# Performance work log

Hardware: AMD Instinct MI355X
Metric: run time of the kernel (lower is better)

Reference implementation:

```python
import jax, jax.numpy as jnp
import numpy as np
from jax import lax

B, D, N, K, POOL = 256, 512, 50000, 32, 1024
ALPHA, BETA, LAMB = 1.0, 1.0, 1e-4
TAU, EPS, DELTA = 0.1, 0.1, 1e-3
SINKHORN_ITERS = 200


def matrix_sqrt(A):
    # differentiable symmetric PSD matrix sqrt via eigendecomposition
    w, v = jnp.linalg.eigh(A)
    w = jnp.clip(w, 0.0)
    return (v * jnp.sqrt(w)) @ v.T


def ridge_cov(M, delta):
    Dm = M.shape[0]
    S = M + (jnp.trace(M) / Dm * delta) * jnp.eye(Dm, dtype=M.dtype)
    return 0.5 * (S + S.T)


def sinkhorn(p, q, C, eps):
    # entropic OT, fixed-iteration Sinkhorn (ot.sinkhorn equivalent)
    Kmat = jnp.exp(-C / eps)
    def step(uv, _):
        u, v = uv
        u = p / (Kmat @ v + 1e-16)
        v = q / (Kmat.T @ u + 1e-16)
        return (u, v), None
    (u, v), _ = lax.scan(step, (jnp.ones_like(p), jnp.ones_like(q)), None, length=SINKHORN_ITERS)
    return u[:, None] * Kmat * v[None, :]


def setup_inputs():
    key = jax.random.key(0)
    k1, k2, k3, k4, k5, k6 = jax.random.split(key, 6)
    return {
        "q_batch": jax.random.normal(k1, (B, D), jnp.float32),
        "q_indices": jax.random.randint(k2, (B,), 0, POOL),
        "W": jax.random.normal(k3, (D, D), jnp.float32) * 0.05,
        "X": jax.random.normal(k4, (N, D), jnp.float32),
        "pre_indices": jax.random.randint(k5, (POOL, K), 0, N),
        "pre_weights": jax.random.uniform(k6, (POOL, K), jnp.float32, 0.1, 1.0),
    }


def _forward(q_batch, W, X, pre_weights, q_indices, pre_indices):
    T = q_batch @ W  # model := single linear layer, T_q_batch [B, D]
    # ---- distribution alignment (2-Wasserstein between Gaussians) ----
    mu_X = X.mean(0)
    Sigma_X = ridge_cov(jnp.cov(X, rowvar=False).astype(X.dtype), DELTA)
    mu_t = T.mean(0)
    Sigma_t = ridge_cov(jnp.cov(T, rowvar=False).astype(T.dtype), max(DELTA, 1e-4))
    term_mean = jnp.sum((mu_t - mu_X) ** 2)
    s_t = matrix_sqrt(Sigma_t)
    M = s_t @ Sigma_X @ s_t
    s_m = matrix_sqrt(0.5 * (M + M.T))
    term_cov = jnp.trace(Sigma_X + Sigma_t - 2.0 * s_m)
    loss_dist = term_mean + jnp.clip(term_cov, 0.0)
    # ---- kNN consistency with entropic OT ----
    T_sg = lax.stop_gradient(T)  # faiss search is on detached queries
    d2 = (T_sg ** 2).sum(1, keepdims=True) - 2.0 * T_sg @ X.T + (X ** 2).sum(1)[None, :]
    _, post_idx = lax.top_k(-d2, K)  # exact brute-force kNN == faiss IndexFlatL2
    Xn = X[post_idx]  # [B, K, D]
    l2 = ((T[:, None, :] - Xn) ** 2).sum(-1)  # [B, K], grads flow through T
    post_w = jax.nn.softmax(-l2 / TAU, axis=1)
    post_w = jnp.clip(post_w, 1e-8)
    post_w = post_w / post_w.sum(1, keepdims=True)
    pre_idx_b = pre_indices[q_indices]  # [B, K]
    pre_w = jnp.clip(pre_weights[q_indices], 1e-8)
    pre_w = pre_w / pre_w.sum(1, keepdims=True)
    # fixed-size support = concat(pre, post) of size 2K; duplicated points cost 0
    # to move between, so OT value matches the deduped-union formulation
    support = jnp.concatenate([pre_idx_b, post_idx], axis=1)  # [B, 2K]
    S = X[support]  # [B, 2K, D]
    sq = (S ** 2).sum(-1)
    C = jnp.clip(sq[:, :, None] + sq[:, None, :] - 2.0 * jnp.einsum('bid,bjd->bij', S, S), 0.0)
    med = jnp.median(C.reshape(C.shape[0], -1), axis=1)
    C = C / (med[:, None, None] + 1e-8)
    zeros = jnp.zeros_like(pre_w)
    p = jnp.concatenate([pre_w, zeros], axis=1)   # pre mass on first K slots
    q = jnp.concatenate([zeros, post_w], axis=1)  # post mass on last K slots
    plans = jax.vmap(lambda pp, qq, cc: sinkhorn(pp, qq, cc, EPS))(p, q, C)
    loss_knn = (plans * C).sum((1, 2)).mean()
    loss_reg = 0.5 * jnp.sum(W ** 2)
    total = ALPHA * loss_dist + BETA * loss_knn + LAMB * loss_reg
    return total, loss_dist, loss_knn


def reference(q_batch, q_indices, W, X, pre_indices, pre_weights):
    return _forward(q_batch, W, X, pre_weights, q_indices, pre_indices)
```

## Files before the change

kernel.cpp:

```cpp
#include <hip/hip_runtime.h>
#include <float.h>
#include <math.h>

#define BB 256
#define DD 512
#define NN 50000
#define KK 32
#define NS_ITERS 11
#define PARTS 8
#define PCH 6250

#define OFF_G     0
#define OFF_SC    262144
#define OFF_CS    262208
#define OFF_CSS   262720
#define ZERO_F    263232
#define OFF_T     263232
#define OFF_TC    394304
#define OFF_P     525376
#define OFF_H     656448
#define OFF_XSQ   723008
#define OFF_RUNI  781200
#define OFF_PW    789392
#define OFF_PRW   797584
#define OFF_D2    805776

#define OFF_UUT   (OFF_G)
#define OFF_TCTC  (OFF_G + 65536)
#define OFF_W     (OFF_G + 131072)
#define OFF_M     (OFF_G + 131328)
#define OFF_MUT   (OFF_G + 200000)

typedef __attribute__((ext_vector_type(8))) short bf16x8;
typedef __attribute__((ext_vector_type(4))) float f32x4;

__device__ __forceinline__ float waveSum(float v) {
#pragma unroll
  for (int off = 32; off > 0; off >>= 1) v += __shfl_xor(v, off);
  return v;
}

__device__ __forceinline__ void cvt_write(float4 v, unsigned short* hi, unsigned short* lo, int sa) {
  unsigned int b0 = __float_as_uint(v.x), b1 = __float_as_uint(v.y);
  unsigned int b2 = __float_as_uint(v.z), b3 = __float_as_uint(v.w);
  unsigned int h0 = b0 & 0xffff0000u, h1 = b1 & 0xffff0000u;
  unsigned int h2 = b2 & 0xffff0000u, h3 = b3 & 0xffff0000u;
  float l0 = v.x - __uint_as_float(h0), l1 = v.y - __uint_as_float(h1);
  float l2 = v.z - __uint_as_float(h2), l3 = v.w - __uint_as_float(h3);
  *(unsigned int*)&hi[sa]     = (h0 >> 16) | h1;
  *(unsigned int*)&hi[sa + 2] = (h2 >> 16) | h3;
  *(unsigned int*)&lo[sa]     = (__float_as_uint(l0) >> 16) | (__float_as_uint(l1) & 0xffff0000u);
  *(unsigned int*)&lo[sa + 2] = (__float_as_uint(l2) >> 16) | (__float_as_uint(l3) & 0xffff0000u);
}

__device__ __forceinline__ void cvt1(float x, unsigned short* hp, unsigned short* lp) {
  unsigned int bb = __float_as_uint(x);
  unsigned int hb = bb & 0xffff0000u;
  float lo = x - __uint_as_float(hb);
  *hp = (unsigned short)(hb >> 16);
  *lp = (unsigned short)(__float_as_uint(lo) >> 16);
}

__global__ void __launch_bounds__(256) k_g64_nn(const float* __restrict__ A,
                                                const float* __restrict__ B,
                                                float* __restrict__ C,
                                                int K, int lda, int ldb, int ldc, float scale,
                                                float* __restrict__ musum) {
  __shared__ float As[64][65], Bs[64][65];
  __shared__ float cp[64];
  int m0 = blockIdx.y * 64, n0 = blockIdx.x * 64;
  int t = threadIdx.x, tr = t >> 4, tc = t & 15;
  float acc[4][4] = {{0.f}};
  for (int k0 = 0; k0 < K; k0 += 64) {
#pragma unroll
    for (int p = 0; p < 16; ++p) {
      int l = t + 256 * p;
      int r = l >> 6, c = l & 63;
      As[r][c] = A[(m0 + r) * lda + k0 + c];
      Bs[r][c] = B[(k0 + r) * ldb + n0 + c];
    }
    __syncthreads();
#pragma unroll 16
    for (int kk = 0; kk < 64; ++kk) {
      float a[4], b[4];
#pragma unroll
      for (int u = 0; u < 4; ++u) a[u] = As[tr + 16 * u][kk];
#pragma unroll
      for (int v = 0; v < 4; ++v) b[v] = Bs[kk][tc + 16 * v];
#pragma unroll
      for (int u = 0; u < 4; ++u)
#pragma unroll
        for (int v = 0; v < 4; ++v) acc[u][v] += a[u] * b[v];
    }
    __syncthreads();
  }
#pragma unroll
  for (int u = 0; u < 4; ++u)
#pragma unroll
    for (int v = 0; v < 4; ++v)
      C[(m0 + tr + 16 * u) * ldc + n0 + tc + 16 * v] = acc[u][v] * scale;
  if (musum != nullptr) {
    if (t < 64) cp[t] = 0.f;
    __syncthreads();
#pragma unroll
    for (int v = 0; v < 4; ++v) {
      float s = 0.f;
#pragma unroll
      for (int u = 0; u < 4; ++u) s += acc[u][v];
      atomicAdd(&cp[tc + 16 * v], s * scale);
    }
    __syncthreads();
    if (t < 64) atomicAdd(&musum[n0 + t], cp[t]);
  }
}

__global__ void __launch_bounds__(256) k_g64_nt(const float* __restrict__ A,
                                                const float* __restrict__ B,
                                                float* __restrict__ C,
                                                int K, int lda, int ldb, int ldc, float scale) {
  __shared__ float As[64][65], Bs[64][65];
  int m0 = blockIdx.y * 64, n0 = blockIdx.x * 64;
  int t = threadIdx.x, tr = t >> 4, tc = t & 15;
  float acc[4][4] = {{0.f}};
  for (int k0 = 0; k0 < K; k0 += 64) {
#pragma unroll
    for (int p = 0; p < 16; ++p) {
      int l = t + 256 * p;
      int r = l >> 6, c = l & 63;
      As[r][c] = A[(m0 + r) * lda + k0 + c];
      Bs[r][c] = B[(n0 + r) * ldb + k0 + c];
    }
    __syncthreads();
#pragma unroll 16
    for (int kk = 0; kk < 64; ++kk) {
      float a[4], b[4];
#pragma unroll
      for (int u = 0; u < 4; ++u) a[u] = As[tr + 16 * u][kk];
#pragma unroll
      for (int v = 0; v < 4; ++v) b[v] = Bs[tc + 16 * v][kk];
#pragma unroll
      for (int u = 0; u < 4; ++u)
#pragma unroll
        for (int v = 0; v < 4; ++v) acc[u][v] += a[u] * b[v];
    }
    __syncthreads();
  }
#pragma unroll
  for (int u = 0; u < 4; ++u)
#pragma unroll
    for (int v = 0; v < 4; ++v)
      C[(m0 + tr + 16 * u) * ldc + n0 + tc + 16 * v] = acc[u][v] * scale;
}

__global__ void __launch_bounds__(256) k_vgemm(const float* __restrict__ T,
                                               const float* __restrict__ X,
                                               float* __restrict__ V,
                                               float* __restrict__ m) {
  __shared__ unsigned short Ah[128 * 72], Al[128 * 72], Bh[128 * 72], Bl[128 * 72];
  __shared__ float colpart[128];
  int bj = blockIdx.x, bi = blockIdx.y;
  int t = threadIdx.x;
  int wave = t >> 6, lane = t & 63;
  int m0 = (wave >> 1) * 64, n0 = (wave & 1) * 64;
  int lrow = lane & 15, lq = lane >> 4;
  int r_ = t >> 4, c4_ = (t & 15) * 4;
  f32x4 acc[4][4] = {};
  float4 pa[8], pb[8];
#pragma unroll
  for (int f = 0; f < 8; ++f) {
    int r = f * 16 + r_;
    pa[f] = *(const float4*)&T[(bi * 128 + r) * 512 + c4_];
    int jg = bj * 128 + r;
    float4 vb = {0.f, 0.f, 0.f, 0.f};
    if (jg < NN) vb = *(const float4*)&X[(size_t)jg * 512 + c4_];
    pb[f] = vb;
  }
  for (int kc = 0; kc < 512; kc += 64) {
#pragma unroll
    for (int f = 0; f < 8; ++f) {
      int sa = (f * 16 + r_) * 72 + c4_;
      cvt_write(pa[f], Ah, Al, sa);
      cvt_write(pb[f], Bh, Bl, sa);
    }
    __syncthreads();
    if (kc < 448) {
      int kn = kc + 64;
#pragma unroll
      for (int f = 0; f < 8; ++f) {
        int r = f * 16 + r_;
        pa[f] = *(const float4*)&T[(bi * 128 + r) * 512 + kn + c4_];
        int jg = bj * 128 + r;
        float4 vb = {0.f, 0.f, 0.f, 0.f};
        if (jg < NN) vb = *(const float4*)&X[(size_t)jg * 512 + kn + c4_];
        pb[f] = vb;
      }
    }
#pragma unroll
    for (int ks = 0; ks < 2; ++ks) {
      int kb = ks * 32 + lq * 8;
      bf16x8 ah[4], al[4], bh[4], bl[4];
#pragma unroll
      for (int mi = 0; mi < 4; ++mi) {
        int ro = (m0 + mi * 16 + lrow) * 72 + kb;
        ah[mi] = *(const bf16x8*)&Ah[ro];
        al[mi] = *(const bf16x8*)&Al[ro];
      }
#pragma unroll
      for (int nj = 0; nj < 4; ++nj) {
        int ro = (n0 + nj * 16 + lrow) * 72 + kb;
        bh[nj] = *(const bf16x8*)&Bh[ro];
        bl[nj] = *(const bf16x8*)&Bl[ro];
      }
#pragma unroll
      for (int mi = 0; mi < 4; ++mi)
#pragma unroll
        for (int nj = 0; nj < 4; ++nj) {
          acc[mi][nj] = __builtin_amdgcn_mfma_f32_16x16x32_bf16(ah[mi], bh[nj], acc[mi][nj], 0, 0, 0);
          acc[mi][nj] = __builtin_amdgcn_mfma_f32_16x16x32_bf16(ah[mi], bl[nj], acc[mi][nj], 0, 0, 0);
          acc[mi][nj] = __builtin_amdgcn_mfma_f32_16x16x32_bf16(al[mi], bh[nj], acc[mi][nj], 0, 0, 0);
        }
    }
    __syncthreads();
  }
  if (t < 128) colpart[t] = 0.f;
  __syncthreads();
#pragma unroll
  for (int mi = 0; mi < 4; ++mi)
#pragma unroll
    for (int nj = 0; nj < 4; ++nj)
#pragma unroll
      for (int r = 0; r < 4; ++r) {
        int row = bi * 128 + m0 + mi * 16 + lq * 4 + r;
        int col = bj * 128 + n0 + nj * 16 + lrow;
        if (col < NN) V[(size_t)row * NN + col] = acc[mi][nj][r];
      }
#pragma unroll
  for (int nj = 0; nj < 4; ++nj) {
    float s = 0.f;
#pragma unroll
    for (int mi = 0; mi < 4; ++mi)
#pragma unroll
      for (int r = 0; r < 4; ++r) s += acc[mi][nj][r];
    atomicAdd(&colpart[n0 + nj * 16 + lrow], s);
  }
  __syncthreads();
  if (t < 128) {
    int col = bj * 128 + t;
    if (col < NN) atomicAdd(&m[col], colpart[t] * (1.0f / 256.0f));
  }
}

__global__ void __launch_bounds__(256) k_uut(const float* __restrict__ V,
                                             const float* __restrict__ m,
                                             float* __restrict__ UUT) {
  __shared__ unsigned short Ah[128 * 72], Al[128 * 72], Bh[128 * 72], Bl[128 * 72];
  __shared__ __align__(16) float ms[1000];
  const int pi_[3] = {0, 0, 1}, pj_[3] = {0, 1, 1};
  int bi = pi_[blockIdx.x], bj = pj_[blockIdx.x];
  bool diag = (bi == bj);
  int j0 = blockIdx.y * 1000, jlim = j0 + 1000;
  int t = threadIdx.x;
  int wave = t >> 6, lane = t & 63;
  int m0 = (wave >> 1) * 64, n0 = (wave & 1) * 64;
  int lrow = lane & 15, lq = lane >> 4;
  int r_ = t >> 4, c4_ = (t & 15) * 4;
  f32x4 acc[4][4] = {};
  if (t < 250) ((float4*)ms)[t] = *(const float4*)&m[j0 + t * 4];
  float4 pa[8], pb[8];
#pragma unroll
  for (int f = 0; f < 8; ++f) {
    int r = f * 16 + r_;
    int jb = j0 + c4_;
    float4 va = {0.f, 0.f, 0.f, 0.f}, vb = {0.f, 0.f, 0.f, 0.f};
    if (jb < jlim) {
      va = *(const float4*)&V[(size_t)(bi * 128 + r) * NN + jb];
      if (!diag) vb = *(const float4*)&V[(size_t)(bj * 128 + r) * NN + jb];
    }
    pa[f] = va; pb[f] = vb;
  }
  __syncthreads();
  const unsigned short* BhP = diag ? (const unsigned short*)Ah : (const unsigned short*)Bh;
  const unsigned short* BlP = diag ? (const unsigned short*)Al : (const unsigned short*)Bl;
  for (int ch = 0; ch < 16; ++ch) {
    int jc = j0 + ch * 64;
#pragma unroll
    for (int f = 0; f < 8; ++f) {
      int sa = (f * 16 + r_) * 72 + c4_;
      int jb = jc + c4_;
      float4 va = pa[f], vb = pb[f];
      if (jb < jlim) {
        float4 mm = *(const float4*)&ms[jb - j0];
        va.x -= mm.x; va.y -= mm.y; va.z -= mm.z; va.w -= mm.w;
        if (!diag) { vb.x -= mm.x; vb.y -= mm.y; vb.z -= mm.z; vb.w -= mm.w; }
      }
      cvt_write(va, Ah, Al, sa);
      if (!diag) cvt_write(vb, Bh, Bl, sa);
    }
    __syncthreads();
    if (ch < 15) {
      int jn = j0 + (ch + 1) * 64;
#pragma unroll
      for (int f = 0; f < 8; ++f) {
        int r = f * 16 + r_;
        int jb = jn + c4_;
        float4 va = {0.f, 0.f, 0.f, 0.f}, vb = {0.f, 0.f, 0.f, 0.f};
        if (jb < jlim) {
          va = *(const float4*)&V[(size_t)(bi * 128 + r) * NN + jb];
          if (!diag) vb = *(const float4*)&V[(size_t)(bj * 128 + r) * NN + jb];
        }
        pa[f] = va; pb[f] = vb;
      }
    }
#pragma unroll
    for (int ks = 0; ks < 2; ++ks) {
      int kb = ks * 32 + lq * 8;
      bf16x8 ah[4], al[4], bh[4], bl[4];
#pragma unroll
      for (int mi = 0; mi < 4; ++mi) {
        int ro = (m0 + mi * 16 + lrow) * 72 + kb;
        ah[mi] = *(const bf16x8*)&Ah[ro];
        al[mi] = *(const bf16x8*)&Al[ro];
      }
#pragma unroll
      for (int nj = 0; nj < 4; ++nj) {
        int ro = (n0 + nj * 16 + lrow) * 72 + kb;
        bh[nj] = *(const bf16x8*)&BhP[ro];
        bl[nj] = *(const bf16x8*)&BlP[ro];
      }
#pragma unroll
      for (int mi = 0; mi < 4; ++mi)
#pragma unroll
        for (int nj = 0; nj < 4; ++nj) {
          acc[mi][nj] = __builtin_amdgcn_mfma_f32_16x16x32_bf16(ah[mi], bh[nj], acc[mi][nj], 0, 0, 0);
          acc[mi][nj] = __builtin_amdgcn_mfma_f32_16x16x32_bf16(ah[mi], bl[nj], acc[mi][nj], 0, 0, 0);
          acc[mi][nj] = __builtin_amdgcn_mfma_f32_16x16x32_bf16(al[mi], bh[nj], acc[mi][nj], 0, 0, 0);
        }
    }
    __syncthreads();
  }
#pragma unroll
  for (int mi = 0; mi < 4; ++mi)
#pragma unroll
    for (int nj = 0; nj < 4; ++nj)
#pragma unroll
      for (int r = 0; r < 4; ++r) {
        int row = bi * 128 + m0 + mi * 16 + lq * 4 + r;
        int col = bj * 128 + n0 + nj * 16 + lrow;
        atomicAdd(&UUT[row * 256 + col], acc[mi][nj][r]);
      }
}

__global__ void __launch_bounds__(256) k_colstatX(const float* __restrict__ X, float* __restrict__ colsum,
                                                  float* __restrict__ colss, float* __restrict__ xsq) {
  __shared__ float shs[512], shq[512];
  int b = blockIdx.x, t = threadIdx.x;
  int wave = t >> 6, lane = t & 63;
  shs[t] = 0.f; shq[t] = 0.f; shs[t + 256] = 0.f; shq[t + 256] = 0.f;
  __syncthreads();
  int c0 = lane * 4;
  float s0 = 0, s1 = 0, s2 = 0, s3 = 0, s4 = 0, s5 = 0, s6 = 0, s7 = 0;
  float q0 = 0, q1 = 0, q2 = 0, q3 = 0, q4 = 0, q5 = 0, q6 = 0, q7 = 0;
  int r0 = b * 200 + wave * 50;
  for (int rr = 0; rr < 50; ++rr) {
    const float* Xr = X + (size_t)(r0 + rr) * 512;
    float4 a = *(const float4*)&Xr[c0];
    float4 c = *(const float4*)&Xr[c0 + 256];
    s0 += a.x; s1 += a.y; s2 += a.z; s3 += a.w;
    s4 += c.x; s5 += c.y; s6 += c.z; s7 += c.w;
    float ax = a.x * a.x, ay = a.y * a.y, az = a.z * a.z, aw = a.w * a.w;
    float cx = c.x * c.x, cy = c.y * c.y, cz = c.z * c.z, cw = c.w * c.w;
    q0 += ax; q1 += ay; q2 += az; q3 += aw;
    q4 += cx; q5 += cy; q6 += cz; q7 += cw;
    float rsq = waveSum(((ax + ay) + (az + aw)) + ((cx + cy) + (cz + cw)));
    if (lane == 0) xsq[r0 + rr] = rsq;
  }
  atomicAdd(&shs[c0 + 0], s0); atomicAdd(&shs[c0 + 1], s1);
  atomicAdd(&shs[c0 + 2], s2); atomicAdd(&shs[c0 + 3], s3);
  atomicAdd(&shs[c0 + 256], s4); atomicAdd(&shs[c0 + 257], s5);
  atomicAdd(&shs[c0 + 258], s6); atomicAdd(&shs[c0 + 259], s7);
  atomicAdd(&shq[c0 + 0], q0); atomicAdd(&shq[c0 + 1], q1);
  atomicAdd(&shq[c0 + 2], q2); atomicAdd(&shq[c0 + 3], q3);
  atomicAdd(&shq[c0 + 256], q4); atomicAdd(&shq[c0 + 257], q5);
  atomicAdd(&shq[c0 + 258], q6); atomicAdd(&shq[c0 + 259], q7);
  __syncthreads();
  atomicAdd(&colsum[t], shs[t]);             atomicAdd(&colss[t], shq[t]);
  atomicAdd(&colsum[t + 256], shs[t + 256]); atomicAdd(&colss[t + 256], shq[t + 256]);
}

__global__ void k_centerT(const float* __restrict__ T, const float* __restrict__ mu,
                          float* __restrict__ Tc, float* __restrict__ scal) {
  __shared__ float red[4];
  int t = threadIdx.x;
  int base = blockIdx.x * 1024;
  float ss = 0.f;
#pragma unroll
  for (int p = 0; p < 4; ++p) {
    int l = base + p * 256 + t;
    float v = T[l] - mu[l & 511] * (1.0f / 256.0f);
    Tc[l] = v;
    ss += v * v;
  }
  ss = waveSum(ss);
  if ((t & 63) == 0) red[t >> 6] = ss;
  __syncthreads();
  if (t == 0) atomicAdd(&scal[0], red[0] + red[1] + red[2] + red[3]);
}

__global__ void k_trCX(const float* __restrict__ colsum, const float* __restrict__ colss,
                       float* __restrict__ scal) {
  __shared__ float red[8];
  int t = threadIdx.x;
  float mu = colsum[t] * (1.0f / 50000.0f);
  float v = (colss[t] - 50000.0f * mu * mu) * (1.0f / 49999.0f);
  v = waveSum(v);
  if ((t & 63) == 0) red[t >> 6] = v;
  __syncthreads();
  if (t == 0) {
    float s = 0;
    for (int i = 0; i < 8; ++i) s += red[i];
    scal[1] = s;
  }
}

__global__ void __launch_bounds__(256) k_wvec(const float* __restrict__ T,
                                              const float* __restrict__ colsum,
                                              float* __restrict__ w, float* __restrict__ scal) {
  __shared__ float cs[512];
  int t = threadIdx.x, lane = t & 63, wv_ = t >> 6;
  cs[t] = colsum[t] * (1.0f / 50000.0f);
  cs[t + 256] = colsum[t + 256] * (1.0f / 50000.0f);
  __syncthreads();
  int rbase = blockIdx.x * 32 + wv_ * 8;
  float tot = 0.f;
  for (int rr = 0; rr < 8; ++rr) {
    int row = rbase + rr;
    float a = 0.f;
#pragma unroll
    for (int d = 0; d < 8; ++d) a += T[row * 512 + lane + 64 * d] * cs[lane + 64 * d];
    a = waveSum(a);
    if (lane == 0) { w[row] = a; tot += a; }
  }
  if (lane == 0) atomicAdd(&scal[6], tot);
}

__global__ void k_hfix(const float* __restrict__ UUT, const float* __restrict__ TcTc,
                       const float* __restrict__ w, const float* __restrict__ scal,
                       float* __restrict__ H) {
  int l = blockIdx.x * 256 + threadIdx.x;
  int i = l >> 8, j = l & 255;
  float u = (i >= 128 && j < 128) ? UUT[j * 256 + i] : UUT[i * 256 + j];
  float rho = scal[1] * (1e-3f / 512.0f);
  float wm = scal[6] * (1.0f / 256.0f);
  float wi = w[i] - wm, wj = w[j] - wm;
  H[l] = (u - 50000.0f * wi * wj) * (1.0f / (49999.0f * 255.0f))
       + rho * TcTc[i * 256 + j] * (1.0f / 255.0f);
}

__global__ void __launch_bounds__(256) k_power(const float* __restrict__ H,
                                               float* __restrict__ scal) {
  __shared__ float v[256], nv[256], red[4];
  int t = threadIdx.x;
  float rt = scal[0] * (1.0f / 255.0f) * (1e-3f / 512.0f);
  v[t] = 1.0f;
  __syncthreads();
  float n2 = 256.0f, n3 = 256.0f;
  for (int it = 0; it < 3; ++it) {
    float s = rt * v[t];
    for (int j = 0; j < 256; ++j) s += H[j * 256 + t] * v[j];
    nv[t] = s;
    float ss = waveSum(s * s);
    if ((t & 63) == 0) red[t >> 6] = ss;
    __syncthreads();
    float norm2 = red[0] + red[1] + red[2] + red[3];
    if (it == 1) n2 = norm2;
    if (it == 2) n3 = norm2;
    v[t] = nv[t];
    __syncthreads();
  }
  float d = H[t * 256 + t] + rt;
#pragma unroll
  for (int off = 32; off > 0; off >>= 1) d = fmaxf(d, __shfl_xor(d, off));
  if ((t & 63) == 0) red[t >> 6] = d;
  __syncthreads();
  if (t == 0) {
    float lam = sqrtf(n3 / n2);
    float md = fmaxf(fmaxf(red[0], red[1]), fmaxf(red[2], red[3]));
    scal[5] = fmaxf(1.3f * lam, md);
  }
}

__global__ void k_nsinit(const float* __restrict__ H, const float* __restrict__ scal,
                         float* __restrict__ Y, float* __restrict__ Z) {
  int l = blockIdx.x * 256 + threadIdx.x;
  int i = l >> 8, j = l & 255;
  float rt = scal[0] * (1.0f / 255.0f) * (1e-3f / 512.0f);
  float inv = 1.0f / scal[5];
  Y[l] = (H[l] + ((i == j) ? rt : 0.f)) * inv;
  Z[l] = (i == j) ? 1.0f : 0.f;
}

__device__ __forceinline__ void ns_mfma_tile(const float* __restrict__ A, const float* __restrict__ B,
                                             const float* __restrict__ D, float* __restrict__ O,
                                             int m0b, int n0b, float dscale, float ascale,
                                             unsigned short* Ah, unsigned short* Al,
                                             unsigned short* Bh, unsigned short* Bl) {
  int t = threadIdx.x, wave = t >> 6, lane = t & 63;
  int m0 = (wave >> 1) * 32, n0 = (wave & 1) * 32;
  int lrow = lane & 15, lq = lane >> 4;
  f32x4 acc[2][2] = {};
  for (int k0 = 0; k0 < 256; k0 += 64) {
#pragma unroll
    for (int f = 0; f < 4; ++f) {
      int lin = f * 256 + t;
      int r = lin >> 4, c4 = (lin & 15) * 4;
      float4 va = *(const float4*)&A[(m0b + r) * 256 + k0 + c4];
      cvt_write(va, Ah, Al, r * 72 + c4);
      float4 vb = *(const float4*)&B[(k0 + r) * 256 + n0b + c4];
      cvt1(vb.x, &Bh[(c4 + 0) * 72 + r], &Bl[(c4 + 0) * 72 + r]);
      cvt1(vb.y, &Bh[(c4 + 1) * 72 + r], &Bl[(c4 + 1) * 72 + r]);
      cvt1(vb.z, &Bh[(c4 + 2) * 72 + r], &Bl[(c4 + 2) * 72 + r]);
      cvt1(vb.w, &Bh[(c4 + 3) * 72 + r], &Bl[(c4 + 3) * 72 + r]);
    }
    __syncthreads();
#pragma unroll
    for (int ks = 0; ks < 2; ++ks) {
      int kb = ks * 32 + lq * 8;
      bf16x8 ah[2], al2[2], bh[2], bl2[2];
#pragma unroll
      for (int mi = 0; mi < 2; ++mi) {
        int ro = (m0 + mi * 16 + lrow) * 72 + kb;
        ah[mi] = *(const bf16x8*)&Ah[ro];
        al2[mi] = *(const bf16x8*)&Al[ro];
      }
#pragma unroll
      for (int nj = 0; nj < 2; ++nj) {
        int ro = (n0 + nj * 16 + lrow) * 72 + kb;
        bh[nj] = *(const bf16x8*)&Bh[ro];
        bl2[nj] = *(const bf16x8*)&Bl[ro];
      }
#pragma unroll
      for (int mi = 0; mi < 2; ++mi)
#pragma unroll
        for (int nj = 0; nj < 2; ++nj) {
          acc[mi][nj] = __builtin_amdgcn_mfma_f32_16x16x32_bf16(ah[mi], bh[nj], acc[mi][nj], 0, 0, 0);
          acc[mi][nj] = __builtin_amdgcn_mfma_f32_16x16x32_bf16(ah[mi], bl2[nj], acc[mi][nj], 0, 0, 0);
          acc[mi][nj] = __builtin_amdgcn_mfma_f32_16x16x32_bf16(al2[mi], bh[nj], acc[mi][nj], 0, 0, 0);
        }
    }
    __syncthreads();
  }
#pragma unroll
  for (int mi = 0; mi < 2; ++mi)
#pragma unroll
    for (int nj = 0; nj < 2; ++nj)
#pragma unroll
      for (int r = 0; r < 4; ++r) {
        int row = m0b + m0 + mi * 16 + lq * 4 + r;
        int col = n0b + n0 + nj * 16 + lrow;
        int idx = row * 256 + col;
        float base = (dscale != 0.f) ? dscale * D[idx] : 0.f;
        O[idx] = base + ascale * acc[mi][nj][r];
      }
}

__global__ void __launch_bounds__(256) k_nsp(const float* __restrict__ Z,
                                             const float* __restrict__ Y,
                                             float* __restrict__ P) {
  __shared__ unsigned short Ah[64 * 72], Al[64 * 72], Bh[64 * 72], Bl[64 * 72];
  ns_mfma_tile(Z, Y, Z, P, blockIdx.y * 64, blockIdx.x * 64, 0.f, 1.0f, Ah, Al, Bh, Bl);
}

__global__ void __launch_bounds__(256) k_nsu(const float* __restrict__ Y, const float* __restrict__ Z,
                                             const float* __restrict__ Pm,
                                             float* __restrict__ Yn, float* __restrict__ Zn) {
  __shared__ unsigned short Ah[64 * 72], Al[64 * 72], Bh[64 * 72], Bl[64 * 72];
  int zz = blockIdx.z;
  if (zz == 0)
    ns_mfma_tile(Y, Pm, Y, Yn, blockIdx.y * 64, blockIdx.x * 64, 1.5f, -0.5f, Ah, Al, Bh, Bl);
  else
    ns_mfma_tile(Pm, Z, Z, Zn, blockIdx.y * 64, blockIdx.x * 64, 1.5f, -0.5f, Ah, Al, Bh, Bl);
}

__global__ void __launch_bounds__(256) k_nsu_diag(const float* __restrict__ Y,
                                                  const float* __restrict__ Pm,
                                                  float* __restrict__ scal) {
  __shared__ unsigned short Ah[64 * 72], Al[64 * 72], Bh[64 * 72], Bl[64 * 72];
  __shared__ float red[4];
  int bi = blockIdx.x;
  int m0b = bi * 64, n0b = bi * 64;
  int t = threadIdx.x, wave = t >> 6, lane = t & 63;
  int m0 = (wave >> 1) * 32, n0 = (wave & 1) * 32;
  int lrow = lane & 15, lq = lane >> 4;
  f32x4 acc[2][2] = {};
  for (int k0 = 0; k0 < 256; k0 += 64) {
#pragma unroll
    for (int f = 0; f < 4; ++f) {
      int lin = f * 256 + t;
      int r = lin >> 4, c4 = (lin & 15) * 4;
      float4 va = *(const float4*)&Y[(m0b + r) * 256 + k0 + c4];
      cvt_write(va, Ah, Al, r * 72 + c4);
      float4 vb = *(const float4*)&Pm[(k0 + r) * 256 + n0b + c4];
      cvt1(vb.x, &Bh[(c4 + 0) * 72 + r], &Bl[(c4 + 0) * 72 + r]);
      cvt1(vb.y, &Bh[(c4 + 1) * 72 + r], &Bl[(c4 + 1) * 72 + r]);
      cvt1(vb.z, &Bh[(c4 + 2) * 72 + r], &Bl[(c4 + 2) * 72 + r]);
      cvt1(vb.w, &Bh[(c4 + 3) * 72 + r], &Bl[(c4 + 3) * 72 + r]);
    }
    __syncthreads();
#pragma unroll
    for (int ks = 0; ks < 2; ++ks) {
      int kb = ks * 32 + lq * 8;
      bf16x8 ah[2], al2[2], bh[2], bl2[2];
#pragma unroll
      for (int mi = 0; mi < 2; ++mi) {
        int ro = (m0 + mi * 16 + lrow) * 72 + kb;
        ah[mi] = *(const bf16x8*)&Ah[ro];
        al2[mi] = *(const bf16x8*)&Al[ro];
      }
#pragma unroll
      for (int nj = 0; nj < 2; ++nj) {
        int ro = (n0 + nj * 16 + lrow) * 72 + kb;
        bh[nj] = *(const bf16x8*)&Bh[ro];
        bl2[nj] = *(const bf16x8*)&Bl[ro];
      }
#pragma unroll
      for (int mi = 0; mi < 2; ++mi)
#pragma unroll
        for (int nj = 0; nj < 2; ++nj) {
          acc[mi][nj] = __builtin_amdgcn_mfma_f32_16x16x32_bf16(ah[mi], bh[nj], acc[mi][nj], 0, 0, 0);
          acc[mi][nj] = __builtin_amdgcn_mfma_f32_16x16x32_bf16(ah[mi], bl2[nj], acc[mi][nj], 0, 0, 0);
          acc[mi][nj] = __builtin_amdgcn_mfma_f32_16x16x32_bf16(al2[mi], bh[nj], acc[mi][nj], 0, 0, 0);
        }
    }
    __syncthreads();
  }
  float lacc = 0.f;
#pragma unroll
  for (int mi = 0; mi < 2; ++mi)
#pragma unroll
    for (int nj = 0; nj < 2; ++nj)
#pragma unroll
      for (int r = 0; r < 4; ++r) {
        int row = m0 + mi * 16 + lq * 4 + r;
        int col = n0 + nj * 16 + lrow;
        if (row == col)
          lacc += 1.5f * Y[(m0b + row) * 256 + n0b + col] - 0.5f * acc[mi][nj][r];
      }
  lacc = waveSum(lacc);
  if ((t & 63) == 0) red[t >> 6] = lacc;
  __syncthreads();
  if (t == 0) atomicAdd(&scal[7], red[0] + red[1] + red[2] + red[3]);
}

__global__ void __launch_bounds__(256) k_topk_part(const float* __restrict__ V,
                                                   const float* __restrict__ xsq,
                                                   float* __restrict__ candv,
                                                   int* __restrict__ candi) {
  __shared__ float bufv[512];
  __shared__ int bufi[512];
  __shared__ int lcount;
  __shared__ float tvs;
  __shared__ int tis;
  int part = blockIdx.x, q = blockIdx.y, t = threadIdx.x;
  int base = part * PCH;
  int lane = t & 63;
  if (t == 0) { lcount = 0; tvs = FLT_MAX; tis = 0x7fffffff; }
  __syncthreads();
  const float* rowV = V + (size_t)q * NN + base;
  const float* xs = xsq + base;

  auto flush = [&]() {
    __syncthreads();
    int c = lcount;
    for (int s = c + t; s < 512; s += 256) { bufv[s] = FLT_MAX; bufi[s] = 0x7fffffff; }
    __syncthreads();
    for (int ssz = 2; ssz <= 512; ssz <<= 1) {
      for (int st = ssz >> 1; st > 0; st >>= 1) {
        int i = 2 * t - (t & (st - 1));
        int j = i + st;
        bool up = ((i & ssz) == 0);
        float a = bufv[i], b = bufv[j];
        int ai = bufi[i], bi2 = bufi[j];
        bool agtb = (a > b) || (a == b && ai > bi2);
        if (agtb == up) { bufv[i] = b; bufv[j] = a; bufi[i] = bi2; bufi[j] = ai; }
        __syncthreads();
      }
    }
    if (t == 0) { lcount = 32; tvs = bufv[31]; tis = bufi[31]; }
    __syncthreads();
  };

  int ntile = (PCH + 255) >> 8;
  for (int tile = 0; tile < ntile; ++tile) {
    int j = tile * 256 + t;
    float val = 0.f; int idx = 0;
    bool pred = false;
    if (j < PCH) {
      val = xs[j] - 2.0f * rowV[j];
      idx = base + j;
      float tv = tvs; int ti = tis;
      pred = (val < tv) || (val == tv && idx < ti);
    }
    unsigned long long mask = __ballot(pred);
    if (mask) {
      int lead = __ffsll((unsigned long long)mask) - 1;
      int cnt = __popcll(mask);
      int basep = 0;
      if (lane == lead) basep = atomicAdd(&lcount, cnt);
      basep = __shfl(basep, lead);
      if (pred) {
        int off = __popcll(mask & ((1ull << lane) - 1ull));
        int slot = basep + off;
        bufv[slot] = val; bufi[slot] = idx;
      }
    }
    __syncthreads();
    if (lcount >= 256) flush();
  }
  flush();
  if (t < 32) {
    candv[(q * PARTS + part) * 32 + t] = bufv[t];
    candi[(q * PARTS + part) * 32 + t] = bufi[t];
  }
}

__global__ void __launch_bounds__(128) k_topk_final(const float* __restrict__ candv,
                                                    const int* __restrict__ candi,
                                                    int* __restrict__ runi) {
  __shared__ float v[256];
  __shared__ int ix[256];
  int q = blockIdx.x, t = threadIdx.x;
  v[t] = candv[q * 256 + t];
  v[t + 128] = candv[q * 256 + t + 128];
  ix[t] = candi[q * 256 + t];
  ix[t + 128] = candi[q * 256 + t + 128];
  __syncthreads();
  for (int ssz = 2; ssz <= 256; ssz <<= 1) {
    for (int st = ssz >> 1; st > 0; st >>= 1) {
      int i = 2 * t - (t & (st - 1));
      int j = i + st;
      bool up = ((i & ssz) == 0);
      float a = v[i], b = v[j];
      int ai = ix[i], bi = ix[j];
      bool agtb = (a > b) || (a == b && ai > bi);
      if (agtb == up) { v[i] = b; v[j] = a; ix[i] = bi; ix[j] = ai; }
      __syncthreads();
    }
  }
  if (t < 32) runi[q * 32 + t] = ix[t];
}

__global__ void __launch_bounds__(256) k_l2soft(const float* __restrict__ T, const float* __restrict__ X,
                                                const int* __restrict__ runi, const int* __restrict__ qidx,
                                                const float* __restrict__ prew, float* __restrict__ postw,
                                                float* __restrict__ prewn) {
  __shared__ float l2s[32];
  int b = blockIdx.x, t = threadIdx.x;
  int wave = t >> 6, lane = t & 63;
  int qi = qidx[b];
  if (wave == 0) {
    float pwv = (lane < 32) ? fmaxf(prew[qi * 32 + lane], 1e-8f) : 0.f;
    float psum = waveSum(pwv);
    if (lane < 32) prewn[b * 32 + lane] = pwv / psum;
  }
  const float* Tb = T + b * 512;
#pragma unroll
  for (int n8 = 0; n8 < 8; ++n8) {
    int n = wave * 8 + n8;
    int nb = runi[b * 32 + n];
    const float* Xr = X + (size_t)nb * 512;
    float acc = 0.f;
#pragma unroll
    for (int d = 0; d < 8; ++d) {
      float df = Tb[lane + 64 * d] - Xr[lane + 64 * d];
      acc += df * df;
    }
    acc = waveSum(acc);
    if (lane == 0) l2s[n] = acc;
  }
  __syncthreads();
  if (wave == 0) {
    float lg = (lane < 32) ? (-l2s[lane] * 10.0f) : -FLT_MAX;
    float mx = lg;
#pragma unroll
    for (int off = 32; off > 0; off >>= 1) mx = fmaxf(mx, __shfl_xor(mx, off));
    float e = (lane < 32) ? expf(lg - mx) : 0.f;
    float es = waveSum(e);
    float wv = e / es;
    wv = fmaxf(wv, 1e-8f);
    float ws2 = (lane < 32) ? wv : 0.f;
    ws2 = waveSum(ws2);
    if (lane < 32) postw[b * 32 + lane] = wv / ws2;
  }
}

__global__ void __launch_bounds__(256) k_batch(const float* __restrict__ X, const int* __restrict__ qidx,
                                               const int* __restrict__ pre_idx, const int* __restrict__ runi,
                                               const float* __restrict__ prewn, const float* __restrict__ postw,
                                               float* __restrict__ scal) {
  __shared__ float G[64][65];
  __shared__ float Cm[64][65];
  __shared__ unsigned short Ah[64 * 72], Al[64 * 72];
  __shared__ int supp[64];
  __shared__ float uuS[32], vvS[32];
  __shared__ float red[4];
  __shared__ float medsh;
  int b = blockIdx.x, t = threadIdx.x;
  int wave = t >> 6, lane = t & 63;
  if (t < 32) supp[t] = pre_idx[qidx[b] * 32 + t];
  else if (t < 64) supp[t] = runi[b * 32 + t - 32];
  __syncthreads();
  {
    int m0 = (wave >> 1) * 32, n0 = (wave & 1) * 32;
    int lrow = lane & 15, lq = lane >> 4;
    int r_ = t >> 4, c4_ = (t & 15) * 4;
    f32x4 acc[2][2] = {};
    float4 pf[4];
#pragma unroll
    for (int f = 0; f < 4; ++f) {
      int r = f * 16 + r_;
      pf[f] = *(const float4*)&X[(size_t)supp[r] * 512 + c4_];
    }
    for (int kc = 0; kc < 512; kc += 64) {
#pragma unroll
      for (int f = 0; f < 4; ++f)
        cvt_write(pf[f], Ah, Al, (f * 16 + r_) * 72 + c4_);
      __syncthreads();
      if (kc < 448) {
        int kn = kc + 64;
#pragma unroll
        for (int f = 0; f < 4; ++f) {
          int r = f * 16 + r_;
          pf[f] = *(const float4*)&X[(size_t)supp[r] * 512 + kn + c4_];
        }
      }
#pragma unroll
      for (int ks = 0; ks < 2; ++ks) {
        int kb = ks * 32 + lq * 8;
        bf16x8 ah[2], al[2], bh[2], bl[2];
#pragma unroll
        for (int mi = 0; mi < 2; ++mi) {
          int ro = (m0 + mi * 16 + lrow) * 72 + kb;
          ah[mi] = *(const bf16x8*)&Ah[ro];
          al[mi] = *(const bf16x8*)&Al[ro];
        }
#pragma unroll
        for (int nj = 0; nj < 2; ++nj) {
          int ro = (n0 + nj * 16 + lrow) * 72 + kb;
          bh[nj] = *(const bf16x8*)&Ah[ro];
          bl[nj] = *(const bf16x8*)&Al[ro];
        }
#pragma unroll
        for (int mi = 0; mi < 2; ++mi)
#pragma unroll
          for (int nj = 0; nj < 2; ++nj) {
            acc[mi][nj] = __builtin_amdgcn_mfma_f32_16x16x32_bf16(ah[mi], bh[nj], acc[mi][nj], 0, 0, 0);
            acc[mi][nj] = __builtin_amdgcn_mfma_f32_16x16x32_bf16(ah[mi], bl[nj], acc[mi][nj], 0, 0, 0);
            acc[mi][nj] = __builtin_amdgcn_mfma_f32_16x16x32_bf16(al[mi], bh[nj], acc[mi][nj], 0, 0, 0);
          }
      }
      __syncthreads();
    }
#pragma unroll
    for (int mi = 0; mi < 2; ++mi)
#pragma unroll
      for (int nj = 0; nj < 2; ++nj)
#pragma unroll
        for (int r = 0; r < 4; ++r)
          G[m0 + mi * 16 + lq * 4 + r][n0 + nj * 16 + lrow] = acc[mi][nj][r];
  }
  __syncthreads();
  for (int l = t; l < 4096; l += 256) {
    int i = l >> 6, j = l & 63;
    Cm[i][j] = fmaxf(G[i][i] + G[j][j] - 2.0f * G[i][j], 0.f);
  }
  __syncthreads();
  if (wave == 0) {
    unsigned int uv2[64];
#pragma unroll
    for (int s = 0; s < 64; ++s)
      uv2[s] = (s < lane) ? (__float_as_uint(Cm[s][lane]) & 0x7fffffffu) : 0xffffffffu;
    unsigned int ans = 0;
    for (int bb2 = 30; bb2 >= 0; --bb2) {
      unsigned int test = ans | (1u << bb2);
      int cnt = 0;
#pragma unroll
      for (int s = 0; s < 64; ++s)
        cnt += __popcll(__ballot(uv2[s] < test));
      if (cnt < 992) ans = test;
    }
    unsigned int cnt2 = 0, mn = 0xffffffffu;
#pragma unroll
    for (int s = 0; s < 64; ++s) {
      unsigned int u2 = uv2[s];
      if (u2 <= ans) cnt2++;
      else mn = (u2 < mn) ? u2 : mn;
    }
#pragma unroll
    for (int off = 32; off > 0; off >>= 1) {
      cnt2 += __shfl_xor(cnt2, off);
      unsigned int m2 = __shfl_xor(mn, off);
      mn = (m2 < mn) ? m2 : mn;
    }
    if (lane == 0) {
      float v992 = __uint_as_float(ans);
      float v993 = (cnt2 >= 993u) ? v992 : __uint_as_float(mn);
      medsh = 0.5f * (v992 + v993) + 1e-8f;
    }
  }
  __syncthreads();
  float inv = 1.0f / medsh;
  for (int l = t; l < 4096; l += 256) {
    int i = l >> 6, j = l & 63;
    float cn = Cm[i][j] * inv;
    Cm[i][j] = cn;
    G[i][j] = expf(-cn * 10.0f);
  }
  __syncthreads();
  if (wave == 0) {
    int half = lane >> 5;
    int l = lane & 31;
    int cb = half * 16;
    float p_l = prewn[b * 32 + l];
    float q_l = postw[b * 32 + l];
    float Kr16[16], Kt16[16];
#pragma unroll
    for (int c2 = 0; c2 < 16; ++c2) Kr16[c2] = G[l][32 + cb + c2];
#pragma unroll
    for (int r2 = 0; r2 < 16; ++r2) Kt16[r2] = G[cb + r2][32 + l];
    float r0 = 0.f;
#pragma unroll
    for (int c2 = 0; c2 < 32; ++c2) r0 += G[l][half * 32 + c2];
    r0 += __shfl_xor(r0, 32);
    float u = p_l / (r0 + 1e-16f);
    float s0 = 0.f, s1 = 0.f, s2 = 0.f, s3 = 0.f;
#pragma unroll
    for (int r2 = 0; r2 < 16; r2 += 4) {
      s0 += Kt16[r2]     * __shfl(u, cb + r2);
      s1 += Kt16[r2 + 1] * __shfl(u, cb + r2 + 1);
      s2 += Kt16[r2 + 2] * __shfl(u, cb + r2 + 2);
      s3 += Kt16[r2 + 3] * __shfl(u, cb + r2 + 3);
    }
    float sv = (s0 + s1) + (s2 + s3);
    sv += __shfl_xor(sv, 32);
    float v = q_l / (sv + 1e-16f);
    float pu = u, pv2 = v;
    float ppu = 0.f, ppv = 0.f;
    for (int it = 1; it < 200; ++it) {
      float a0 = 0.f, a1 = 0.f, a2 = 0.f, a3 = 0.f;
#pragma unroll
      for (int c2 = 0; c2 < 16; c2 += 4) {
        a0 += Kr16[c2]     * __shfl(v, cb + c2);
        a1 += Kr16[c2 + 1] * __shfl(v, cb + c2 + 1);
        a2 += Kr16[c2 + 2] * __shfl(v, cb + c2 + 2);
        a3 += Kr16[c2 + 3] * __shfl(v, cb + c2 + 3);
      }
      float au = (a0 + a1) + (a2 + a3);
      au += __shfl_xor(au, 32);
      u = p_l / (au + 1e-16f);
      a0 = 0.f; a1 = 0.f; a2 = 0.f; a3 = 0.f;
#pragma unroll
      for (int r2 = 0; r2 < 16; r2 += 4) {
        a0 += Kt16[r2]     * __shfl(u, cb + r2);
        a1 += Kt16[r2 + 1] * __shfl(u, cb + r2 + 1);
        a2 += Kt16[r2 + 2] * __shfl(u, cb + r2 + 2);
        a3 += Kt16[r2 + 3] * __shfl(u, cb + r2 + 3);
      }
      float bv = (a0 + a1) + (a2 + a3);
      bv += __shfl_xor(bv, 32);
      v = q_l / (bv + 1e-16f);
      if (__all(u == pu && v == pv2)) break;
      if (it >= 2 && __all(u == ppu && v == ppv)) {
        if ((199 - it) & 1) { u = pu; v = pv2; }
        break;
      }
      ppu = pu; ppv = pv2; pu = u; pv2 = v;
    }
    if (t < 32) { uuS[t] = u; vvS[t] = v; }
  }
  __syncthreads();
  float lacc = 0.f;
#pragma unroll
  for (int q8 = 0; q8 < 4; ++q8) {
    int l = q8 * 256 + t;
    int i = l >> 5, j = l & 31;
    lacc += uuS[i] * G[i][32 + j] * vvS[j] * Cm[i][32 + j];
  }
  lacc = waveSum(lacc);
  if ((t & 63) == 0) red[t >> 6] = lacc;
  __syncthreads();
  if (t == 0)
    atomicAdd(&scal[3], (red[0] + red[1] + red[2] + red[3]) * (1.0f / 256.0f));
}

__global__ void k_wreg(const float* __restrict__ W, float* __restrict__ scal) {
  __shared__ float red[4];
  int t = threadIdx.x;
  int base = blockIdx.x * 2048;
  float ss = 0.f;
#pragma unroll
  for (int p = 0; p < 8; ++p) {
    float v = W[base + p * 256 + t];
    ss += v * v;
  }
  ss = waveSum(ss);
  if ((t & 63) == 0) red[t >> 6] = ss;
  __syncthreads();
  if (t == 0) atomicAdd(&scal[4], red[0] + red[1] + red[2] + red[3]);
}

__global__ void k_combine(const float* __restrict__ mu_t, const float* __restrict__ colsum,
                          const float* __restrict__ scal, float* __restrict__ out) {
  __shared__ float red[8];
  int t = threadIdx.x;
  float dm = mu_t[t] * (1.0f / 256.0f) - colsum[t] * (1.0f / 50000.0f);
  float v = dm * dm;
  v = waveSum(v);
  if ((t & 63) == 0) red[t >> 6] = v;
  __syncthreads();
  if (t == 0) {
    float term_mean = 0.f;
    for (int i = 0; i < 8; ++i) term_mean += red[i];
    float trCT = scal[0] * (1.0f / 255.0f);
    float trCX = scal[1];
    float rt = scal[0] * (1.0f / 255.0f) * (1e-3f / 512.0f);
    float S = sqrtf(scal[5]) * scal[7] + 256.0f * sqrtf(rt);
    float term_cov = trCX * 1.001f + trCT * 1.001f - 2.0f * S;
    term_cov = fmaxf(term_cov, 0.f);
    float loss_dist = term_mean + term_cov;
    float loss_knn = scal[3];
    float loss_reg = 0.5f * scal[4];
    out[0] = loss_dist + loss_knn + 1e-4f * loss_reg;
    out[1] = loss_dist;
    out[2] = loss_knn;
  }
}

extern "C" void kernel_launch(void* const* d_in, const int* in_sizes, int n_in,
                              void* d_out, int out_size, void* d_ws, size_t ws_size,
                              hipStream_t stream) {
  const float* q = (const float*)d_in[0];
  const int* qidx = (const int*)d_in[1];
  const float* W = (const float*)d_in[2];
  const float* X = (const float*)d_in[3];
  const int* pre_idx = (const int*)d_in[4];
  const float* prew = (const float*)d_in[5];
  float* out = (float*)d_out;
  float* ws = (float*)d_ws;

  float* scal = ws + OFF_SC;
  float* colsum = ws + OFF_CS;
  float* colss = ws + OFF_CSS;
  float* T = ws + OFF_T;
  float* Tc = ws + OFF_TC;
  float* H = ws + OFF_H;
  float* mu_t = ws + OFF_MUT;
  float* xsq = ws + OFF_XSQ;
  int* runi = (int*)(ws + OFF_RUNI);
  float* postw = ws + OFF_PW;
  float* prewn = ws + OFF_PRW;
  float* V = ws + OFF_D2;
  float* UUT = ws + OFF_UUT;
  float* TcTc = ws + OFF_TCTC;
  float* wv = ws + OFF_W;
  float* m = ws + OFF_M;
  float* candv = ws + OFF_P;
  int* candi = (int*)(ws + OFF_P + 65536);

  hipMemsetAsync(d_ws, 0, (size_t)ZERO_F * 4, stream);

  k_g64_nn<<<dim3(8, 4), 256, 0, stream>>>(q, W, T, 512, 512, 512, 512, 1.0f, mu_t);
  k_colstatX<<<250, 256, 0, stream>>>(X, colsum, colss, xsq);
  k_centerT<<<128, 256, 0, stream>>>(T, mu_t, Tc, scal);
  k_trCX<<<1, 512, 0, stream>>>(colsum, colss, scal);
  k_vgemm<<<dim3(391, 2), 256, 0, stream>>>(T, X, V, m);
  k_topk_part<<<dim3(PARTS, 256), 256, 0, stream>>>(V, xsq, candv, candi);
  k_topk_final<<<256, 128, 0, stream>>>(candv, candi, runi);
  k_g64_nt<<<dim3(4, 4), 256, 0, stream>>>(Tc, Tc, TcTc, 512, 512, 512, 256, 1.0f);
  k_wvec<<<8, 256, 0, stream>>>(T, colsum, wv, scal);
  k_uut<<<dim3(3, 50), 256, 0, stream>>>(V, m, UUT);
  {
    float* Y = ws + OFF_TC;
    float* Z = ws + OFF_TC + 65536;
    float* Y2 = ws + OFF_P;
    float* Z2 = ws + OFF_P + 65536;
    float* Pm = ws + OFF_G;
    k_hfix<<<256, 256, 0, stream>>>(UUT, TcTc, wv, scal, H);
    k_power<<<1, 256, 0, stream>>>(H, scal);
    k_nsinit<<<256, 256, 0, stream>>>(H, scal, Y, Z);
    for (int it = 0; it < NS_ITERS - 1; ++it) {
      k_nsp<<<dim3(4, 4), 256, 0, stream>>>(Z, Y, Pm);
      k_nsu<<<dim3(4, 4, 2), 256, 0, stream>>>(Y, Z, Pm, Y2, Z2);
      float* tmp = Y; Y = Y2; Y2 = tmp;
      tmp = Z; Z = Z2; Z2 = tmp;
    }
    k_nsp<<<dim3(4, 4), 256, 0, stream>>>(Z, Y, Pm);
    k_nsu_diag<<<4, 256, 0, stream>>>(Y, Pm, scal);
  }
  k_l2soft<<<256, 256, 0, stream>>>(T, X, runi, qidx, prew, postw, prewn);
  k_batch<<<256, 256, 0, stream>>>(X, qidx, pre_idx, runi, prewn, postw, scal);
  k_wreg<<<128, 256, 0, stream>>>(W, scal);
  k_combine<<<1, 512, 0, stream>>>(mu_t, colsum, scal, out);
}
```

Measured before the change: 959.7 us.

## Fuse small kernels, radix-select median, and drop diag branch in UUT

```diff
diff --git a/kernel.cpp b/kernel.cpp
--- a/kernel.cpp
+++ b/kernel.cpp
@@ -257,7 +257,6 @@
   __shared__ __align__(16) float ms[1000];
   const int pi_[3] = {0, 0, 1}, pj_[3] = {0, 1, 1};
   int bi = pi_[blockIdx.x], bj = pj_[blockIdx.x];
-  bool diag = (bi == bj);
   int j0 = blockIdx.y * 1000, jlim = j0 + 1000;
   int t = threadIdx.x;
   int wave = t >> 6, lane = t & 63;
@@ -274,13 +273,11 @@
     float4 va = {0.f, 0.f, 0.f, 0.f}, vb = {0.f, 0.f, 0.f, 0.f};
     if (jb < jlim) {
       va = *(const float4*)&V[(size_t)(bi * 128 + r) * NN + jb];
-      if (!diag) vb = *(const float4*)&V[(size_t)(bj * 128 + r) * NN + jb];
+      vb = *(const float4*)&V[(size_t)(bj * 128 + r) * NN + jb];
     }
     pa[f] = va; pb[f] = vb;
   }
   __syncthreads();
-  const unsigned short* BhP = diag ? (const unsigned short*)Ah : (const unsigned short*)Bh;
-  const unsigned short* BlP = diag ? (const unsigned short*)Al : (const unsigned short*)Bl;
   for (int ch = 0; ch < 16; ++ch) {
     int jc = j0 + ch * 64;
 #pragma unroll
@@ -291,10 +288,10 @@
       if (jb < jlim) {
         float4 mm = *(const float4*)&ms[jb - j0];
         va.x -= mm.x; va.y -= mm.y; va.z -= mm.z; va.w -= mm.w;
-        if (!diag) { vb.x -= mm.x; vb.y -= mm.y; vb.z -= mm.z; vb.w -= mm.w; }
+        vb.x -= mm.x; vb.y -= mm.y; vb.z -= mm.z; vb.w -= mm.w;
       }
       cvt_write(va, Ah, Al, sa);
-      if (!diag) cvt_write(vb, Bh, Bl, sa);
+      cvt_write(vb, Bh, Bl, sa);
     }
     __syncthreads();
     if (ch < 15) {
@@ -306,7 +303,7 @@
         float4 va = {0.f, 0.f, 0.f, 0.f}, vb = {0.f, 0.f, 0.f, 0.f};
         if (jb < jlim) {
           va = *(const float4*)&V[(size_t)(bi * 128 + r) * NN + jb];
-          if (!diag) vb = *(const float4*)&V[(size_t)(bj * 128 + r) * NN + jb];
+          vb = *(const float4*)&V[(size_t)(bj * 128 + r) * NN + jb];
         }
         pa[f] = va; pb[f] = vb;
       }
@@ -324,8 +321,8 @@
 #pragma unroll
       for (int nj = 0; nj < 4; ++nj) {
         int ro = (n0 + nj * 16 + lrow) * 72 + kb;
-        bh[nj] = *(const bf16x8*)&BhP[ro];
-        bl[nj] = *(const bf16x8*)&BlP[ro];
+        bh[nj] = *(const bf16x8*)&Bh[ro];
+        bl[nj] = *(const bf16x8*)&Bl[ro];
       }
 #pragma unroll
       for (int mi = 0; mi < 4; ++mi)
@@ -406,27 +403,25 @@
   if (t == 0) atomicAdd(&scal[0], red[0] + red[1] + red[2] + red[3]);
 }
 
-__global__ void k_trCX(const float* __restrict__ colsum, const float* __restrict__ colss,
-                       float* __restrict__ scal) {
-  __shared__ float red[8];
-  int t = threadIdx.x;
-  float mu = colsum[t] * (1.0f / 50000.0f);
-  float v = (colss[t] - 50000.0f * mu * mu) * (1.0f / 49999.0f);
-  v = waveSum(v);
-  if ((t & 63) == 0) red[t >> 6] = v;
-  __syncthreads();
-  if (t == 0) {
-    float s = 0;
-    for (int i = 0; i < 8; ++i) s += red[i];
-    scal[1] = s;
-  }
-}
-
-__global__ void __launch_bounds__(256) k_wvec(const float* __restrict__ T,
-                                              const float* __restrict__ colsum,
-                                              float* __restrict__ w, float* __restrict__ scal) {
+__global__ void __launch_bounds__(256) k_wvec_trcx(const float* __restrict__ T,
+                                                   const float* __restrict__ colsum,
+                                                   const float* __restrict__ colss,
+                                                   float* __restrict__ w, float* __restrict__ scal) {
   __shared__ float cs[512];
+  __shared__ float red[4];
   int t = threadIdx.x, lane = t & 63, wv_ = t >> 6;
+  if (blockIdx.x == 8) {
+    float s = 0.f;
+    for (int cc = t; cc < 512; cc += 256) {
+      float mu = colsum[cc] * (1.0f / 50000.0f);
+      s += (colss[cc] - 50000.0f * mu * mu) * (1.0f / 49999.0f);
+    }
+    s = waveSum(s);
+    if (lane == 0) red[wv_] = s;
+    __syncthreads();
+    if (t == 0) scal[1] = red[0] + red[1] + red[2] + red[3];
+    return;
+  }
   cs[t] = colsum[t] * (1.0f / 50000.0f);
   cs[t + 256] = colsum[t + 256] * (1.0f / 50000.0f);
   __syncthreads();
@@ -723,40 +718,36 @@
   }
 }
 
-__global__ void __launch_bounds__(128) k_topk_final(const float* __restrict__ candv,
-                                                    const int* __restrict__ candi,
-                                                    int* __restrict__ runi) {
+__global__ void __launch_bounds__(256) k_l2soft(const float* __restrict__ candv,
+                                                const int* __restrict__ candi,
+                                                const float* __restrict__ T, const float* __restrict__ X,
+                                                const int* __restrict__ qidx,
+                                                const float* __restrict__ prew, float* __restrict__ postw,
+                                                float* __restrict__ prewn, int* __restrict__ runi) {
   __shared__ float v[256];
   __shared__ int ix[256];
-  int q = blockIdx.x, t = threadIdx.x;
-  v[t] = candv[q * 256 + t];
-  v[t + 128] = candv[q * 256 + t + 128];
-  ix[t] = candi[q * 256 + t];
-  ix[t + 128] = candi[q * 256 + t + 128];
-  __syncthreads();
-  for (int ssz = 2; ssz <= 256; ssz <<= 1) {
-    for (int st = ssz >> 1; st > 0; st >>= 1) {
-      int i = 2 * t - (t & (st - 1));
-      int j = i + st;
-      bool up = ((i & ssz) == 0);
-      float a = v[i], b = v[j];
-      int ai = ix[i], bi = ix[j];
-      bool agtb = (a > b) || (a == b && ai > bi);
-      if (agtb == up) { v[i] = b; v[j] = a; ix[i] = bi; ix[j] = ai; }
-      __syncthreads();
-    }
-  }
-  if (t < 32) runi[q * 32 + t] = ix[t];
-}
-
-__global__ void __launch_bounds__(256) k_l2soft(const float* __restrict__ T, const float* __restrict__ X,
-                                                const int* __restrict__ runi, const int* __restrict__ qidx,
-                                                const float* __restrict__ prew, float* __restrict__ postw,
-                                                float* __restrict__ prewn) {
   __shared__ float l2s[32];
   int b = blockIdx.x, t = threadIdx.x;
   int wave = t >> 6, lane = t & 63;
   int qi = qidx[b];
+  v[t] = candv[b * 256 + t];
+  ix[t] = candi[b * 256 + t];
+  for (int ssz = 2; ssz <= 256; ssz <<= 1) {
+    for (int st = ssz >> 1; st > 0; st >>= 1) {
+      __syncthreads();
+      if (t < 128) {
+        int i = 2 * t - (t & (st - 1));
+        int j = i + st;
+        bool up = ((i & ssz) == 0);
+        float a = v[i], bb2 = v[j];
+        int ai = ix[i], bi = ix[j];
+        bool agtb = (a > bb2) || (a == bb2 && ai > bi);
+        if (agtb == up) { v[i] = bb2; v[j] = a; ix[i] = bi; ix[j] = ai; }
+      }
+    }
+  }
+  __syncthreads();
+  if (t < 32) runi[b * 32 + t] = ix[t];
   if (wave == 0) {
     float pwv = (lane < 32) ? fmaxf(prew[qi * 32 + lane], 1e-8f) : 0.f;
     float psum = waveSum(pwv);
@@ -766,7 +757,7 @@
 #pragma unroll
   for (int n8 = 0; n8 < 8; ++n8) {
     int n = wave * 8 + n8;
-    int nb = runi[b * 32 + n];
+    int nb = ix[n];
     const float* Xr = X + (size_t)nb * 512;
     float acc = 0.f;
 #pragma unroll
@@ -804,10 +795,16 @@
   __shared__ float uuS[32], vvS[32];
   __shared__ float red[4];
   __shared__ float medsh;
+  __shared__ unsigned int hist[256];
+  __shared__ unsigned int wtot[4];
+  __shared__ unsigned int selp;
+  __shared__ int selk;
+  __shared__ unsigned int cw[4], mw[4];
   int b = blockIdx.x, t = threadIdx.x;
   int wave = t >> 6, lane = t & 63;
   if (t < 32) supp[t] = pre_idx[qidx[b] * 32 + t];
   else if (t < 64) supp[t] = runi[b * 32 + t - 32];
+  if (t == 0) { selp = 0u; selk = 992; }
   __syncthreads();
   {
     int m0 = (wave >> 1) * 32, n0 = (wave & 1) * 32;
@@ -874,40 +871,69 @@
     Cm[i][j] = fmaxf(G[i][i] + G[j][j] - 2.0f * G[i][j], 0.f);
   }
   __syncthreads();
-  if (wave == 0) {
-    unsigned int uv2[64];
-#pragma unroll
-    for (int s = 0; s < 64; ++s)
-      uv2[s] = (s < lane) ? (__float_as_uint(Cm[s][lane]) & 0x7fffffffu) : 0xffffffffu;
-    unsigned int ans = 0;
-    for (int bb2 = 30; bb2 >= 0; --bb2) {
-      unsigned int test = ans | (1u << bb2);
-      int cnt = 0;
-#pragma unroll
-      for (int s = 0; s < 64; ++s)
-        cnt += __popcll(__ballot(uv2[s] < test));
-      if (cnt < 992) ans = test;
-    }
-    unsigned int cnt2 = 0, mn = 0xffffffffu;
-#pragma unroll
-    for (int s = 0; s < 64; ++s) {
-      unsigned int u2 = uv2[s];
-      if (u2 <= ans) cnt2++;
-      else mn = (u2 < mn) ? u2 : mn;
+  for (int pass = 0; pass < 4; ++pass) {
+    int shift = 24 - 8 * pass;
+    hist[t] = 0u;
+    __syncthreads();
+    for (int l = t; l < 4096; l += 256) {
+      int i = l >> 6, j = l & 63;
+      if (i < j) {
+        unsigned int u = __float_as_uint(Cm[i][j]) & 0x7fffffffu;
+        bool match = (pass == 0) || (((u ^ selp) >> (shift + 8)) == 0u);
+        if (match) atomicAdd(&hist[(u >> shift) & 255], 1u);
+      }
+    }
+    __syncthreads();
+    unsigned int h = hist[t];
+    unsigned int c = h;
+#pragma unroll
+    for (int off = 1; off < 64; off <<= 1) {
+      unsigned int n = __shfl_up(c, off);
+      if ((t & 63) >= off) c += n;
+    }
+    if ((t & 63) == 63) wtot[t >> 6] = c;
+    __syncthreads();
+    unsigned int offw = 0;
+    for (int w2 = 0; w2 < (t >> 6); ++w2) offw += wtot[w2];
+    c += offw;
+    int k = selk;
+    if ((int)c >= k && (int)(c - h) < k) {
+      selk = k - (int)(c - h);
+      selp = selp | ((unsigned int)t << shift);
+    }
+    __syncthreads();
+  }
+  {
+    unsigned int target = selp;
+    unsigned int cnt = 0, mn = 0xffffffffu;
+    for (int l = t; l < 4096; l += 256) {
+      int i = l >> 6, j = l & 63;
+      if (i < j) {
+        unsigned int u = __float_as_uint(Cm[i][j]) & 0x7fffffffu;
+        if (u <= target) cnt++;
+        else mn = (u < mn) ? u : mn;
+      }
     }
 #pragma unroll
     for (int off = 32; off > 0; off >>= 1) {
-      cnt2 += __shfl_xor(cnt2, off);
+      cnt += __shfl_xor(cnt, off);
       unsigned int m2 = __shfl_xor(mn, off);
       mn = (m2 < mn) ? m2 : mn;
     }
-    if (lane == 0) {
-      float v992 = __uint_as_float(ans);
-      float v993 = (cnt2 >= 993u) ? v992 : __uint_as_float(mn);
+    if (lane == 0) { cw[wave] = cnt; mw[wave] = mn; }
+    __syncthreads();
+    if (t == 0) {
+      unsigned int ct = cw[0] + cw[1] + cw[2] + cw[3];
+      unsigned int mt = mw[0];
+      mt = (mw[1] < mt) ? mw[1] : mt;
+      mt = (mw[2] < mt) ? mw[2] : mt;
+      mt = (mw[3] < mt) ? mw[3] : mt;
+      float v992 = __uint_as_float(target);
+      float v993 = (ct >= 993u) ? v992 : __uint_as_float(mt);
       medsh = 0.5f * (v992 + v993) + 1e-8f;
     }
-  }
-  __syncthreads();
+    __syncthreads();
+  }
   float inv = 1.0f / medsh;
   for (int l = t; l < 4096; l += 256) {
     int i = l >> 6, j = l & 63;
@@ -1071,12 +1097,11 @@
   k_g64_nn<<<dim3(8, 4), 256, 0, stream>>>(q, W, T, 512, 512, 512, 512, 1.0f, mu_t);
   k_colstatX<<<250, 256, 0, stream>>>(X, colsum, colss, xsq);
   k_centerT<<<128, 256, 0, stream>>>(T, mu_t, Tc, scal);
-  k_trCX<<<1, 512, 0, stream>>>(colsum, colss, scal);
   k_vgemm<<<dim3(391, 2), 256, 0, stream>>>(T, X, V, m);
   k_topk_part<<<dim3(PARTS, 256), 256, 0, stream>>>(V, xsq, candv, candi);
-  k_topk_final<<<256, 128, 0, stream>>>(candv, candi, runi);
+  k_l2soft<<<256, 256, 0, stream>>>(candv, candi, T, X, qidx, prew, postw, prewn, runi);
   k_g64_nt<<<dim3(4, 4), 256, 0, stream>>>(Tc, Tc, TcTc, 512, 512, 512, 256, 1.0f);
-  k_wvec<<<8, 256, 0, stream>>>(T, colsum, wv, scal);
+  k_wvec_trcx<<<9, 256, 0, stream>>>(T, colsum, colss, wv, scal);
   k_uut<<<dim3(3, 50), 256, 0, stream>>>(V, m, UUT);
   {
     float* Y = ws + OFF_TC;
@@ -1096,7 +1121,6 @@
     k_nsp<<<dim3(4, 4), 256, 0, stream>>>(Z, Y, Pm);
     k_nsu_diag<<<4, 256, 0, stream>>>(Y, Pm, scal);
   }
-  k_l2soft<<<256, 256, 0, stream>>>(T, X, runi, qidx, prew, postw, prewn);
   k_batch<<<256, 256, 0, stream>>>(X, qidx, pre_idx, runi, prewn, postw, scal);
   k_wreg<<<128, 256, 0, stream>>>(W, scal);
   k_combine<<<1, 512, 0, stream>>>(mu_t, colsum, scal, out);
```

Measured after the change: 905.3 us. -5.7%, faster.
